# Kernel tuning notes

Hardware: AMD Instinct MI355X
Metric: run time of the kernel (lower is better)

The kernel has to match this reference:

```python
import jax, jax.numpy as jnp
import numpy as np

DIM = 512
HEADS = 8
D_HEAD = 64
INNER_FF = 4 * DIM  # 2048
EPS = 1e-5
SCALE = D_HEAD ** -0.5


def _layernorm(x, w, b):
    x = x.astype(jnp.float32)
    mu = jnp.mean(x, axis=-1, keepdims=True)
    var = jnp.mean(jnp.square(x - mu), axis=-1, keepdims=True)
    return (x - mu) * jax.lax.rsqrt(var + EPS) * w + b


def _l2_attn(x, wq, bq, wv, bv, wo, bo):
    # x: [B, N, DIM]. k = q (context is ignored in the original module).
    b, n, _ = x.shape
    q = (x @ wq + bq).reshape(b, n, HEADS, D_HEAD).transpose(0, 2, 1, 3)  # b h n d
    v = (x @ wv + bv).reshape(b, n, HEADS, D_HEAD).transpose(0, 2, 1, 3)
    q = q.astype(jnp.float32)
    AB = jnp.einsum('bhid,bhjd->bhij', q, q)          # [b,h,n,n]
    AA = jnp.sum(jnp.square(q), axis=-1)               # [b,h,n]
    sim = -(AA[..., :, None] - 2.0 * AB + AA[..., None, :]) * SCALE
    attn = jax.nn.softmax(sim, axis=-1)
    out = jnp.einsum('bhij,bhjd->bhid', attn, v)       # [b,h,n,d]
    out = out.transpose(0, 2, 1, 3).reshape(b, n, HEADS * D_HEAD)
    return out @ wo + bo


def _geglu_ff(x, w1, b1, w2, b2):
    h = x @ w1 + b1                      # [B, N, 2*INNER_FF]
    a, gate = jnp.split(h, 2, axis=-1)
    return (a * jax.nn.gelu(gate, approximate=False)) @ w2 + b2


def setup_inputs() -> dict:
    key = jax.random.key(0)
    ks = jax.random.split(key, 24)
    s = 0.02
    d = {'x': jax.random.normal(ks[0], (4, 2048, DIM), jnp.float32)}
    # layernorms
    d['sa_norm_w'] = jnp.ones((DIM,), jnp.float32)
    d['sa_norm_b'] = jnp.zeros((DIM,), jnp.float32)
    d['ca_norm_w'] = jnp.ones((DIM,), jnp.float32)
    d['ca_norm_b'] = jnp.zeros((DIM,), jnp.float32)
    d['ff_norm_w'] = jnp.ones((DIM,), jnp.float32)
    d['ff_norm_b'] = jnp.zeros((DIM,), jnp.float32)
    # attn1 (self)
    d['a1_wq'] = jax.random.normal(ks[1], (DIM, DIM), jnp.float32) * s
    d['a1_bq'] = jnp.zeros((DIM,), jnp.float32)
    d['a1_wv'] = jax.random.normal(ks[2], (DIM, DIM), jnp.float32) * s
    d['a1_bv'] = jnp.zeros((DIM,), jnp.float32)
    d['a1_wo'] = jax.random.normal(ks[3], (DIM, DIM), jnp.float32) * s
    d['a1_bo'] = jnp.zeros((DIM,), jnp.float32)
    # attn2 (cross, but k=q and v from x in original code)
    d['a2_wq'] = jax.random.normal(ks[4], (DIM, DIM), jnp.float32) * s
    d['a2_bq'] = jnp.zeros((DIM,), jnp.float32)
    d['a2_wv'] = jax.random.normal(ks[5], (DIM, DIM), jnp.float32) * s
    d['a2_bv'] = jnp.zeros((DIM,), jnp.float32)
    d['a2_wo'] = jax.random.normal(ks[6], (DIM, DIM), jnp.float32) * s
    d['a2_bo'] = jnp.zeros((DIM,), jnp.float32)
    # GEGLU FFN
    d['ff_w1'] = jax.random.normal(ks[7], (DIM, 2 * INNER_FF), jnp.float32) * s
    d['ff_b1'] = jnp.zeros((2 * INNER_FF,), jnp.float32)
    d['ff_w2'] = jax.random.normal(ks[8], (INNER_FF, DIM), jnp.float32) * s
    d['ff_b2'] = jnp.zeros((DIM,), jnp.float32)
    return d


def reference(x, sa_norm_w, sa_norm_b, ca_norm_w, ca_norm_b, ff_norm_w, ff_norm_b,
              a1_wq, a1_bq, a1_wv, a1_bv, a1_wo, a1_bo,
              a2_wq, a2_bq, a2_wv, a2_bv, a2_wo, a2_bo,
              ff_w1, ff_b1, ff_w2, ff_b2):
    x = _l2_attn(_layernorm(x, sa_norm_w, sa_norm_b), a1_wq, a1_bq, a1_wv, a1_bv, a1_wo, a1_bo) + x
    x = _l2_attn(_layernorm(x, ca_norm_w, ca_norm_b), a2_wq, a2_bq, a2_wv, a2_bv, a2_wo, a2_bo) + x
    x = _geglu_ff(_layernorm(x, ff_norm_w, ff_norm_b), ff_w1, ff_b1, ff_w2, ff_b2) + x
    return x
```

## Files before the change

### kernel.cpp

```cpp
#include <hip/hip_runtime.h>
#include <hip/hip_bf16.h>


typedef short bf16x8 __attribute__((ext_vector_type(8)));
typedef float f32x4 __attribute__((ext_vector_type(4)));
typedef unsigned short u16;
typedef unsigned int u32;

__device__ __forceinline__ float bf2f(u16 u) {
    return __uint_as_float(((u32)u) << 16);
}
__device__ __forceinline__ u16 f2bf(float f) {
    u32 u = __float_as_uint(f);
    u32 rb = ((u >> 16) & 1u) + 0x7fffu;
    return (u16)((u + rb) >> 16);
}
__device__ __forceinline__ float gelu_fast(float x) {
    float y = 1.5957691216f * (x + 0.044715f * x * x * x);
    return x / (1.f + __expf(-y));
}
__device__ __forceinline__ void gl2lds16(const u16* g, u16* l) {
    __builtin_amdgcn_global_load_lds(
        (const __attribute__((address_space(1))) void*)(unsigned long long)(uintptr_t)g,
        (__attribute__((address_space(3))) void*)(unsigned long long)(uintptr_t)l,
        16, 0, 0);
}

struct TArgs {
    const float* src[8];
    u16* dst[8];
    int R[8], C[8];
    int start[9];
};
__global__ __launch_bounds__(256) void transpose_multi(TArgs a) {
    __shared__ float tile[32][33];
    int bid = blockIdx.x;
    int s = 0;
    while (bid >= a.start[s + 1]) s++;
    int local = bid - a.start[s];
    int R = a.R[s], C = a.C[s];
    int tx = C >> 5;
    int bx = local % tx, by = local / tx;
    const float* in = a.src[s];
    u16* out = a.dst[s];
    int t = threadIdx.x;
    int c = t & 31, r0 = (t >> 5) * 4;
#pragma unroll
    for (int i = 0; i < 4; i++)
        tile[r0 + i][c] = in[(size_t)(by * 32 + r0 + i) * C + bx * 32 + c];
    __syncthreads();
#pragma unroll
    for (int i = 0; i < 4; i++)
        out[(size_t)(bx * 32 + r0 + i) * R + by * 32 + c] = f2bf(tile[c][r0 + i]);
}

__global__ __launch_bounds__(256) void ln_kernel(const float* __restrict__ x,
                                                 const float* __restrict__ w,
                                                 const float* __restrict__ b,
                                                 u16* __restrict__ out) {
    int row = blockIdx.x, t = threadIdx.x;
    const float* xr = x + (size_t)row * 512;
    float2 v = *(const float2*)(xr + t * 2);
    float s1 = v.x + v.y;
    float s2 = v.x * v.x + v.y * v.y;
#pragma unroll
    for (int m = 1; m < 64; m <<= 1) {
        s1 += __shfl_xor(s1, m);
        s2 += __shfl_xor(s2, m);
    }
    __shared__ float r1[4], r2[4];
    int wave = t >> 6, lane = t & 63;
    if (lane == 0) { r1[wave] = s1; r2[wave] = s2; }
    __syncthreads();
    float tot1 = r1[0] + r1[1] + r1[2] + r1[3];
    float tot2 = r2[0] + r2[1] + r2[2] + r2[3];
    float mu = tot1 * (1.f / 512.f);
    float var = tot2 * (1.f / 512.f) - mu * mu;
    float rs = rsqrtf(var + 1e-5f);
    float2 wv = *(const float2*)(w + t * 2);
    float2 bv = *(const float2*)(b + t * 2);
    float o0 = (v.x - mu) * rs * wv.x + bv.x;
    float o1 = (v.y - mu) * rs * wv.y + bv.y;
    u32 pack = (u32)f2bf(o0) | ((u32)f2bf(o1) << 16);
    *(u32*)(out + (size_t)row * 512 + t * 2) = pack;
}

__global__ __launch_bounds__(256) void gemm_ff1(const u16* __restrict__ A,
                                                const u16* __restrict__ BT,
                                                const float* __restrict__ bias,
                                                u16* __restrict__ gout,
                                                int K) {
    __shared__ u16 As[2][128 * 32];
    __shared__ u16 Bs[2][128 * 32];
    int t = threadIdx.x;
    int wave = t >> 6, lane = t & 63, quad = lane >> 4, l16 = lane & 15;
    int m0 = blockIdx.x * 128, n0 = blockIdx.y * 64;
    f32x4 aacc[2][4], gacc[2][4];
#pragma unroll
    for (int i = 0; i < 2; i++)
#pragma unroll
        for (int j = 0; j < 4; j++) {
            aacc[i][j] = (f32x4){0.f, 0.f, 0.f, 0.f};
            gacc[i][j] = (f32x4){0.f, 0.f, 0.f, 0.f};
        }
    const u16* Ag = A + (size_t)(m0 + wave * 32 + (lane >> 2)) * K + (lane & 3) * 8;
    int brow = (wave < 2) ? (n0 + wave * 32) : (2048 + n0 + (wave - 2) * 32);
    const u16* Bg = BT + (size_t)(brow + (lane >> 2)) * K + (lane & 3) * 8;
    int lo = wave * 32 * 32;
    const size_t rstep = (size_t)16 * K;
    gl2lds16(Ag, &As[0][lo]);
    gl2lds16(Ag + rstep, &As[0][lo + 16 * 32]);
    gl2lds16(Bg, &Bs[0][lo]);
    gl2lds16(Bg + rstep, &Bs[0][lo + 16 * 32]);
    int buf = 0;
    for (int k0 = 0; k0 < K; k0 += 32, buf ^= 1) {
        int kn = (k0 + 32 < K) ? (k0 + 32) : k0;
        int nb = buf ^ 1;
        asm volatile("s_waitcnt lgkmcnt(0)\n\ts_barrier" ::: "memory");
        gl2lds16(Ag + kn, &As[nb][lo]);
        gl2lds16(Ag + kn + rstep, &As[nb][lo + 16 * 32]);
        gl2lds16(Bg + kn, &Bs[nb][lo]);
        gl2lds16(Bg + kn + rstep, &Bs[nb][lo + 16 * 32]);
        asm volatile("s_waitcnt vmcnt(4)\n\ts_barrier" ::: "memory");
        bf16x8 a[2];
#pragma unroll
        for (int i = 0; i < 2; i++)
            a[i] = *(const bf16x8*)&As[buf][(wave * 32 + i * 16 + l16) * 32 + quad * 8];
#pragma unroll
        for (int j = 0; j < 4; j++) {
            bf16x8 ba = *(const bf16x8*)&Bs[buf][(j * 16 + l16) * 32 + quad * 8];
            bf16x8 bg = *(const bf16x8*)&Bs[buf][(64 + j * 16 + l16) * 32 + quad * 8];
#pragma unroll
            for (int i = 0; i < 2; i++) {
                aacc[i][j] = __builtin_amdgcn_mfma_f32_16x16x32_bf16(a[i], ba, aacc[i][j], 0, 0, 0);
                gacc[i][j] = __builtin_amdgcn_mfma_f32_16x16x32_bf16(a[i], bg, gacc[i][j], 0, 0, 0);
            }
        }
    }
    asm volatile("s_waitcnt vmcnt(0)" ::: "memory");
    int row_base = m0 + wave * 32 + quad * 4;
#pragma unroll
    for (int j = 0; j < 4; j++) {
        int col = n0 + j * 16 + l16;
        float ba = bias[col];
        float bg = bias[2048 + col];
#pragma unroll
        for (int i = 0; i < 2; i++) {
#pragma unroll
            for (int r = 0; r < 4; r++) {
                int row = row_base + i * 16 + r;
                float av = aacc[i][j][r] + ba;
                float gv = gacc[i][j][r] + bg;
                gout[(size_t)row * 2048 + col] = f2bf(av * gelu_fast(gv));
            }
        }
    }
}

template <int MODE>
__global__ __launch_bounds__(256) void gemm_rect(const u16* __restrict__ A,
                                                 const u16* __restrict__ BT,
                                                 const float* __restrict__ bias,
                                                 const float* __restrict__ bias2,
                                                 const float* __restrict__ res,
                                                 float* __restrict__ outf,
                                                 u16* __restrict__ outb,
                                                 u16* __restrict__ outb2,
                                                 float* __restrict__ aa,
                                                 int M, int N, int K) {
    __shared__ u16 As[2][128 * 32];
    __shared__ u16 Bs[2][64 * 32];
    int t = threadIdx.x;
    int wave = t >> 6, lane = t & 63, quad = lane >> 4, l16 = lane & 15;
    int m0 = blockIdx.x * 128, n0 = blockIdx.y * 64;
    f32x4 acc[2][4];
#pragma unroll
    for (int i = 0; i < 2; i++)
#pragma unroll
        for (int j = 0; j < 4; j++) acc[i][j] = (f32x4){0.f, 0.f, 0.f, 0.f};
    const u16* Ag = A + (size_t)(m0 + wave * 32 + (lane >> 2)) * K + (lane & 3) * 8;
    const u16* Bg = BT + (size_t)(n0 + wave * 16 + (lane >> 2)) * K + (lane & 3) * 8;
    int loA = wave * 32 * 32;
    int loB = wave * 16 * 32;
    const size_t rstep = (size_t)16 * K;
    gl2lds16(Ag, &As[0][loA]);
    gl2lds16(Ag + rstep, &As[0][loA + 16 * 32]);
    gl2lds16(Bg, &Bs[0][loB]);
    int buf = 0;
    for (int k0 = 0; k0 < K; k0 += 32, buf ^= 1) {
        int kn = (k0 + 32 < K) ? (k0 + 32) : k0;
        int nb = buf ^ 1;
        asm volatile("s_waitcnt lgkmcnt(0)\n\ts_barrier" ::: "memory");
        gl2lds16(Ag + kn, &As[nb][loA]);
        gl2lds16(Ag + kn + rstep, &As[nb][loA + 16 * 32]);
        gl2lds16(Bg + kn, &Bs[nb][loB]);
        asm volatile("s_waitcnt vmcnt(3)\n\ts_barrier" ::: "memory");
        bf16x8 a[2], b[4];
#pragma unroll
        for (int i = 0; i < 2; i++)
            a[i] = *(const bf16x8*)&As[buf][(wave * 32 + i * 16 + l16) * 32 + quad * 8];
#pragma unroll
        for (int j = 0; j < 4; j++)
            b[j] = *(const bf16x8*)&Bs[buf][(j * 16 + l16) * 32 + quad * 8];
#pragma unroll
        for (int i = 0; i < 2; i++)
#pragma unroll
            for (int j = 0; j < 4; j++)
                acc[i][j] = __builtin_amdgcn_mfma_f32_16x16x32_bf16(a[i], b[j], acc[i][j], 0, 0, 0);
    }
    asm volatile("s_waitcnt vmcnt(0)" ::: "memory");
    int row_base = m0 + wave * 32 + quad * 4;
    float ssq[2][4];
#pragma unroll
    for (int i = 0; i < 2; i++)
#pragma unroll
        for (int r = 0; r < 4; r++) ssq[i][r] = 0.f;
#pragma unroll
    for (int j = 0; j < 4; j++) {
        int col = n0 + j * 16 + l16;
        float bv;
        if (MODE == 4) bv = (col < 512) ? bias[col] : bias2[col - 512];
        else bv = bias[col];
#pragma unroll
        for (int i = 0; i < 2; i++) {
            int rowA = row_base + i * 16;
            if (MODE == 4) {
                if (col < 512) {
                    int hh = col >> 6, d = col & 63;
#pragma unroll
                    for (int r = 0; r < 4; r++) {
                        int row = rowA + r;
                        float v = acc[i][j][r] + bv;
                        ssq[i][r] += v * v;
                        outb[((size_t)((row >> 11) * 8 + hh) * 2048 + (row & 2047)) * 64 + d] = f2bf(v);
                    }
                } else {
                    int c2 = col - 512;
                    int hh = c2 >> 6, d = c2 & 63;
                    int n = rowA & 2047;
                    int a4 = (n >> 2) & 7;
                    int ncol = (n & ~31) + ((a4 & 3) << 3) + ((a4 >> 2) << 2);
                    u32 plo = (u32)f2bf(acc[i][j][0] + bv) | ((u32)f2bf(acc[i][j][1] + bv) << 16);
                    u32 phi = (u32)f2bf(acc[i][j][2] + bv) | ((u32)f2bf(acc[i][j][3] + bv) << 16);
                    uint2 pk; pk.x = plo; pk.y = phi;
                    *(uint2*)&outb2[((size_t)((rowA >> 11) * 8 + hh) * 64 + d) * 2048 + ncol] = pk;
                }
            } else {
#pragma unroll
                for (int r = 0; r < 4; r++) {
                    size_t idx = (size_t)(rowA + r) * N + col;
                    outf[idx] = acc[i][j][r] + bv + res[idx];
                }
            }
        }
    }
    if (MODE == 4 && n0 < 512) {
        int hh = n0 >> 6;
#pragma unroll
        for (int i = 0; i < 2; i++) {
#pragma unroll
            for (int r = 0; r < 4; r++) {
                float s = ssq[i][r];
                s += __shfl_xor(s, 1); s += __shfl_xor(s, 2);
                s += __shfl_xor(s, 4); s += __shfl_xor(s, 8);
                if (l16 == 0) {
                    int row = row_base + i * 16 + r;
                    aa[(size_t)((row >> 11) * 8 + hh) * 2048 + (row & 2047)] = s * 0.18033688f;
                }
            }
        }
    }
}

__global__ __launch_bounds__(256) void attn_mfma(const u16* __restrict__ qbuf,
                                                 const u16* __restrict__ vtp,
                                                 const float* __restrict__ aas,
                                                 u16* __restrict__ out) {
    __shared__ u16 L[2][16384];
    int bid = blockIdx.x;
    int bh = bid & 31;
    int itile = bid >> 5;
    const u16* qb = qbuf + (size_t)bh * 2048 * 64;
    const u16* vtb = vtp + (size_t)bh * 64 * 2048;
    const float* aab = aas + (size_t)bh * 2048;
    int t = threadIdx.x;
    int wave = t >> 6, lane = t & 63, quad = lane >> 4, l16 = lane & 15;
    int sw7 = l16 & 7;
    int ibase = itile * 128 + wave * 32;

    bf16x8 qf[2][2];
    f32x4 O[2][4];
    float lr[2] = {0.f, 0.f};
#pragma unroll
    for (int st = 0; st < 2; st++) {
        const u16* qr = qb + (size_t)(ibase + st * 16 + l16) * 64;
        qf[st][0] = *(const bf16x8*)(qr + quad * 8);
        qf[st][1] = *(const bf16x8*)(qr + 32 + quad * 8);
#pragma unroll
        for (int nt = 0; nt < 4; nt++) O[st][nt] = (f32x4){0.f, 0.f, 0.f, 0.f};
    }

    int qrow[4], qcs[4], qwof[4], vrow[4], vsl[4], vwof[4];
#pragma unroll
    for (int k = 0; k < 4; k++) {
        int s = t + k * 256;
        qrow[k] = s >> 3; qcs[k] = s & 7;
        qwof[k] = qrow[k] * 64 + 8 * (qcs[k] ^ (qrow[k] & 7));
        vrow[k] = s >> 4; vsl[k] = s & 15;
        vwof[k] = 8192 + vrow[k] * 128 + 8 * ((vsl[k] & 8) | ((vsl[k] & 7) ^ (vrow[k] & 7)));
    }
#pragma unroll
    for (int k = 0; k < 4; k++) {
        *(uint4*)&L[0][qwof[k]] = *(const uint4*)(qb + (size_t)qrow[k] * 64 + qcs[k] * 8);
        *(uint4*)&L[0][vwof[k]] = *(const uint4*)(vtb + (size_t)vrow[k] * 2048 + vsl[k] * 8);
    }
    __syncthreads();

    const float C0 = 0.36067376f;
    for (int it = 0; it < 16; ++it) {
        int cur = it & 1;
        int j0 = it << 7;
        uint4 pq[4], pv[4];
        bool more = (it + 1 < 16);
        if (more) {
            int j0n = j0 + 128;
#pragma unroll
            for (int k = 0; k < 4; k++) {
                pq[k] = *(const uint4*)(qb + (size_t)(j0n + qrow[k]) * 64 + qcs[k] * 8);
                pv[k] = *(const uint4*)(vtb + (size_t)vrow[k] * 2048 + j0n + vsl[k] * 8);
            }
        }
        const u16* Q = &L[cur][0];
        const u16* V = &L[cur][8192];
#pragma unroll
        for (int c = 0; c < 4; c++) {
            int r10 = c * 32 + l16, r20 = c * 32 + 16 + l16;
            bf16x8 a10 = *(const bf16x8*)&Q[r10 * 64 + 8 * (quad ^ sw7)];
            bf16x8 a11 = *(const bf16x8*)&Q[r10 * 64 + 8 * ((4 + quad) ^ sw7)];
            bf16x8 a20 = *(const bf16x8*)&Q[r20 * 64 + 8 * (quad ^ sw7)];
            bf16x8 a21 = *(const bf16x8*)&Q[r20 * 64 + 8 * ((4 + quad) ^ sw7)];
            f32x4 s0[2], s1[2];
            __builtin_amdgcn_s_setprio(1);
#pragma unroll
            for (int st = 0; st < 2; st++) {
                f32x4 z = {0.f, 0.f, 0.f, 0.f};
                s0[st] = __builtin_amdgcn_mfma_f32_16x16x32_bf16(a10, qf[st][0], z, 0, 0, 0);
                s0[st] = __builtin_amdgcn_mfma_f32_16x16x32_bf16(a11, qf[st][1], s0[st], 0, 0, 0);
                s1[st] = __builtin_amdgcn_mfma_f32_16x16x32_bf16(a20, qf[st][0], z, 0, 0, 0);
                s1[st] = __builtin_amdgcn_mfma_f32_16x16x32_bf16(a21, qf[st][1], s1[st], 0, 0, 0);
            }
            __builtin_amdgcn_s_setprio(0);
            float4 aav0 = *(const float4*)(aab + j0 + c * 32 + quad * 4);
            float4 aav1 = *(const float4*)(aab + j0 + c * 32 + 16 + quad * 4);
            bf16x8 pa[2];
#pragma unroll
            for (int st = 0; st < 2; st++) {
                float p0 = __builtin_amdgcn_exp2f(fmaf(s0[st][0], C0, -aav0.x));
                float p1 = __builtin_amdgcn_exp2f(fmaf(s0[st][1], C0, -aav0.y));
                float p2 = __builtin_amdgcn_exp2f(fmaf(s0[st][2], C0, -aav0.z));
                float p3 = __builtin_amdgcn_exp2f(fmaf(s0[st][3], C0, -aav0.w));
                float p4 = __builtin_amdgcn_exp2f(fmaf(s1[st][0], C0, -aav1.x));
                float p5 = __builtin_amdgcn_exp2f(fmaf(s1[st][1], C0, -aav1.y));
                float p6 = __builtin_amdgcn_exp2f(fmaf(s1[st][2], C0, -aav1.z));
                float p7 = __builtin_amdgcn_exp2f(fmaf(s1[st][3], C0, -aav1.w));
                lr[st] += (p0 + p1 + p2 + p3) + (p4 + p5 + p6 + p7);
                u32* pu = (u32*)&pa[st];
                pu[0] = __builtin_amdgcn_perm(__float_as_uint(p1), __float_as_uint(p0), 0x07060302u);
                pu[1] = __builtin_amdgcn_perm(__float_as_uint(p3), __float_as_uint(p2), 0x07060302u);
                pu[2] = __builtin_amdgcn_perm(__float_as_uint(p5), __float_as_uint(p4), 0x07060302u);
                pu[3] = __builtin_amdgcn_perm(__float_as_uint(p7), __float_as_uint(p6), 0x07060302u);
            }
            __builtin_amdgcn_s_setprio(1);
#pragma unroll
            for (int nt = 0; nt < 4; nt++) {
                int sl = c * 4 + quad;
                bf16x8 vf = *(const bf16x8*)&V[(nt * 16 + l16) * 128 + 8 * ((sl & 8) | ((sl & 7) ^ sw7))];
                O[0][nt] = __builtin_amdgcn_mfma_f32_16x16x32_bf16(pa[0], vf, O[0][nt], 0, 0, 0);
                O[1][nt] = __builtin_amdgcn_mfma_f32_16x16x32_bf16(pa[1], vf, O[1][nt], 0, 0, 0);
            }
            __builtin_amdgcn_s_setprio(0);
        }
        if (more) {
            u16* D = &L[cur ^ 1][0];
#pragma unroll
            for (int k = 0; k < 4; k++) {
                *(uint4*)&D[qwof[k]] = pq[k];
                *(uint4*)&D[vwof[k]] = pv[k];
            }
        }
        __syncthreads();
    }

    int b = bh >> 3, h = bh & 7;
#pragma unroll
    for (int st = 0; st < 2; st++) {
        float l = lr[st];
        l += __shfl_xor(l, 16);
        l += __shfl_xor(l, 32);
        float inv = 1.f / l;
#pragma unroll
        for (int r = 0; r < 4; r++) {
            float invr = __shfl(inv, quad * 4 + r);
            size_t row = (size_t)(b * 2048 + ibase + st * 16 + quad * 4 + r);
            u16* o = out + row * 512 + h * 64 + l16;
            o[0]  = f2bf(O[st][0][r] * invr);
            o[16] = f2bf(O[st][1][r] * invr);
            o[32] = f2bf(O[st][2][r] * invr);
            o[48] = f2bf(O[st][3][r] * invr);
        }
    }
}

extern "C" void kernel_launch(void* const* d_in, const int* in_sizes, int n_in,
                              void* d_out, int out_size, void* d_ws, size_t ws_size,
                              hipStream_t stream) {
    const float* x      = (const float*)d_in[0];
    const float* sa_w   = (const float*)d_in[1];
    const float* sa_b   = (const float*)d_in[2];
    const float* ca_w   = (const float*)d_in[3];
    const float* ca_b   = (const float*)d_in[4];
    const float* ffn_w  = (const float*)d_in[5];
    const float* ffn_b  = (const float*)d_in[6];
    const float* a1_wq  = (const float*)d_in[7];
    const float* a1_bq  = (const float*)d_in[8];
    const float* a1_wv  = (const float*)d_in[9];
    const float* a1_bv  = (const float*)d_in[10];
    const float* a1_wo  = (const float*)d_in[11];
    const float* a1_bo  = (const float*)d_in[12];
    const float* a2_wq  = (const float*)d_in[13];
    const float* a2_bq  = (const float*)d_in[14];
    const float* a2_wv  = (const float*)d_in[15];
    const float* a2_bv  = (const float*)d_in[16];
    const float* a2_wo  = (const float*)d_in[17];
    const float* a2_bo  = (const float*)d_in[18];
    const float* ff_w1  = (const float*)d_in[19];
    const float* ff_b1  = (const float*)d_in[20];
    const float* ff_w2  = (const float*)d_in[21];
    const float* ff_b2  = (const float*)d_in[22];

    char* ws = (char*)d_ws;
    const size_t MB = 1ull << 20;
    float* x_res   = (float*)(ws);
    u16* xn        = (u16*)(ws + 16 * MB);
    u16* wT_a1qv   = (u16*)(ws + 24 * MB);
    u16* wT_a2qv   = (u16*)(ws + 25 * MB);
    u16* wT_a1o    = (u16*)(ws + 26 * MB);
    u16* wT_a2o    = (u16*)(ws + 26 * MB + 512 * 1024);
    u16* wT_ff1    = (u16*)(ws + 27 * MB);
    u16* wT_ff2    = (u16*)(ws + 31 * MB);
    u16* qbuf      = (u16*)(ws + 34 * MB);
    u16* vtp       = (u16*)(ws + 42 * MB);
    float* aab     = (float*)(ws + 50 * MB);
    u16* attn_o    = (u16*)(ws + 51 * MB);
    u16* gbuf      = (u16*)(ws + 60 * MB);

    (void)in_sizes; (void)n_in; (void)out_size; (void)ws_size;

    TArgs ta;
    ta.src[0] = a1_wq; ta.dst[0] = wT_a1qv;               ta.R[0] = 512;  ta.C[0] = 512;
    ta.src[1] = a1_wv; ta.dst[1] = wT_a1qv + 512 * 512;   ta.R[1] = 512;  ta.C[1] = 512;
    ta.src[2] = a2_wq; ta.dst[2] = wT_a2qv;               ta.R[2] = 512;  ta.C[2] = 512;
    ta.src[3] = a2_wv; ta.dst[3] = wT_a2qv + 512 * 512;   ta.R[3] = 512;  ta.C[3] = 512;
    ta.src[4] = a1_wo; ta.dst[4] = wT_a1o;                ta.R[4] = 512;  ta.C[4] = 512;
    ta.src[5] = a2_wo; ta.dst[5] = wT_a2o;                ta.R[5] = 512;  ta.C[5] = 512;
    ta.src[6] = ff_w1; ta.dst[6] = wT_ff1;                ta.R[6] = 512;  ta.C[6] = 4096;
    ta.src[7] = ff_w2; ta.dst[7] = wT_ff2;                ta.R[7] = 2048; ta.C[7] = 512;
    ta.start[0] = 0;
    for (int s = 0; s < 8; s++)
        ta.start[s + 1] = ta.start[s] + (ta.C[s] >> 5) * (ta.R[s] >> 5);
    transpose_multi<<<ta.start[8], 256, 0, stream>>>(ta);

    ln_kernel<<<8192, 256, 0, stream>>>(x, sa_w, sa_b, xn);
    gemm_rect<4><<<dim3(64, 16), 256, 0, stream>>>(xn, wT_a1qv, a1_bq, a1_bv, nullptr, nullptr, qbuf, vtp, aab, 8192, 1024, 512);
    attn_mfma<<<512, 256, 0, stream>>>(qbuf, vtp, aab, attn_o);
    gemm_rect<2><<<dim3(64, 8), 256, 0, stream>>>(attn_o, wT_a1o, a1_bo, nullptr, x, x_res, nullptr, nullptr, nullptr, 8192, 512, 512);

    ln_kernel<<<8192, 256, 0, stream>>>(x_res, ca_w, ca_b, xn);
    gemm_rect<4><<<dim3(64, 16), 256, 0, stream>>>(xn, wT_a2qv, a2_bq, a2_bv, nullptr, nullptr, qbuf, vtp, aab, 8192, 1024, 512);
    attn_mfma<<<512, 256, 0, stream>>>(qbuf, vtp, aab, attn_o);
    gemm_rect<2><<<dim3(64, 8), 256, 0, stream>>>(attn_o, wT_a2o, a2_bo, nullptr, x_res, x_res, nullptr, nullptr, nullptr, 8192, 512, 512);

    ln_kernel<<<8192, 256, 0, stream>>>(x_res, ffn_w, ffn_b, xn);
    gemm_ff1<<<dim3(64, 32), 256, 0, stream>>>(xn, wT_ff1, ff_b1, gbuf, 512);
    gemm_rect<2><<<dim3(64, 8), 256, 0, stream>>>(gbuf, wT_ff2, ff_b2, nullptr, x_res, (float*)d_out, nullptr, nullptr, nullptr, 8192, 512, 2048);
}
```

Before: 399.4 us.

## Split attention key range in two and add a combine kernel

The attention kernel now splits the 2048-key range into two halves, launching 1024 blocks instead of 512, each streaming 64-key tiles with a smaller LDS footprint. Each block writes unnormalized fp32 partial outputs and row sums to workspace. A new combine kernel adds the two halves, normalizes, and writes bf16 output. The aim is better CU occupancy and more parallelism (512 blocks on 256 CUs), paid for with extra fp32 partial-result traffic and an extra launch per attention layer.

```diff
diff --git a/kernel.cpp b/kernel.cpp
--- a/kernel.cpp
+++ b/kernel.cpp
@@ -275,11 +275,14 @@
 __global__ __launch_bounds__(256) void attn_mfma(const u16* __restrict__ qbuf,
                                                  const u16* __restrict__ vtp,
                                                  const float* __restrict__ aas,
-                                                 u16* __restrict__ out) {
-    __shared__ u16 L[2][16384];
+                                                 float* __restrict__ opart,
+                                                 float* __restrict__ lrpart) {
+    __shared__ u16 L[2][8192];
     int bid = blockIdx.x;
     int bh = bid & 31;
-    int itile = bid >> 5;
+    int js = (bid >> 5) & 1;
+    int itile = bid >> 6;
+    int jbase = js << 10;
     const u16* qb = qbuf + (size_t)bh * 2048 * 64;
     const u16* vtb = vtp + (size_t)bh * 64 * 2048;
     const float* aab = aas + (size_t)bh * 2048;
@@ -300,40 +303,42 @@
         for (int nt = 0; nt < 4; nt++) O[st][nt] = (f32x4){0.f, 0.f, 0.f, 0.f};
     }
 
-    int qrow[4], qcs[4], qwof[4], vrow[4], vsl[4], vwof[4];
-#pragma unroll
-    for (int k = 0; k < 4; k++) {
-        int s = t + k * 256;
-        qrow[k] = s >> 3; qcs[k] = s & 7;
-        qwof[k] = qrow[k] * 64 + 8 * (qcs[k] ^ (qrow[k] & 7));
-        vrow[k] = s >> 4; vsl[k] = s & 15;
-        vwof[k] = 8192 + vrow[k] * 128 + 8 * ((vsl[k] & 8) | ((vsl[k] & 7) ^ (vrow[k] & 7)));
-    }
-#pragma unroll
-    for (int k = 0; k < 4; k++) {
-        *(uint4*)&L[0][qwof[k]] = *(const uint4*)(qb + (size_t)qrow[k] * 64 + qcs[k] * 8);
-        *(uint4*)&L[0][vwof[k]] = *(const uint4*)(vtb + (size_t)vrow[k] * 2048 + vsl[k] * 8);
+    int r1 = t >> 3, cs = t & 7;
+    int swof = 8 * (cs ^ (r1 & 7));
+    int qwof1 = r1 * 64 + swof;
+    int qwof2 = (r1 + 32) * 64 + swof;
+    int vwof1 = 4096 + qwof1;
+    int vwof2 = 4096 + qwof2;
+
+    {
+        uint4 pq1 = *(const uint4*)(qb + (size_t)(jbase + r1) * 64 + cs * 8);
+        uint4 pq2 = *(const uint4*)(qb + (size_t)(jbase + r1 + 32) * 64 + cs * 8);
+        uint4 pv1 = *(const uint4*)(vtb + (size_t)r1 * 2048 + jbase + cs * 8);
+        uint4 pv2 = *(const uint4*)(vtb + (size_t)(r1 + 32) * 2048 + jbase + cs * 8);
+        *(uint4*)&L[0][qwof1] = pq1;
+        *(uint4*)&L[0][qwof2] = pq2;
+        *(uint4*)&L[0][vwof1] = pv1;
+        *(uint4*)&L[0][vwof2] = pv2;
     }
     __syncthreads();
 
     const float C0 = 0.36067376f;
     for (int it = 0; it < 16; ++it) {
         int cur = it & 1;
-        int j0 = it << 7;
-        uint4 pq[4], pv[4];
+        int j0 = jbase + (it << 6);
+        uint4 pq1, pq2, pv1, pv2;
         bool more = (it + 1 < 16);
         if (more) {
-            int j0n = j0 + 128;
-#pragma unroll
-            for (int k = 0; k < 4; k++) {
-                pq[k] = *(const uint4*)(qb + (size_t)(j0n + qrow[k]) * 64 + qcs[k] * 8);
-                pv[k] = *(const uint4*)(vtb + (size_t)vrow[k] * 2048 + j0n + vsl[k] * 8);
-            }
+            int j0n = j0 + 64;
+            pq1 = *(const uint4*)(qb + (size_t)(j0n + r1) * 64 + cs * 8);
+            pq2 = *(const uint4*)(qb + (size_t)(j0n + r1 + 32) * 64 + cs * 8);
+            pv1 = *(const uint4*)(vtb + (size_t)r1 * 2048 + j0n + cs * 8);
+            pv2 = *(const uint4*)(vtb + (size_t)(r1 + 32) * 2048 + j0n + cs * 8);
         }
         const u16* Q = &L[cur][0];
-        const u16* V = &L[cur][8192];
-#pragma unroll
-        for (int c = 0; c < 4; c++) {
+        const u16* V = &L[cur][4096];
+#pragma unroll
+        for (int c = 0; c < 2; c++) {
             int r10 = c * 32 + l16, r20 = c * 32 + 16 + l16;
             bf16x8 a10 = *(const bf16x8*)&Q[r10 * 64 + 8 * (quad ^ sw7)];
             bf16x8 a11 = *(const bf16x8*)&Q[r10 * 64 + 8 * ((4 + quad) ^ sw7)];
@@ -373,8 +378,7 @@
             __builtin_amdgcn_s_setprio(1);
 #pragma unroll
             for (int nt = 0; nt < 4; nt++) {
-                int sl = c * 4 + quad;
-                bf16x8 vf = *(const bf16x8*)&V[(nt * 16 + l16) * 128 + 8 * ((sl & 8) | ((sl & 7) ^ sw7))];
+                bf16x8 vf = *(const bf16x8*)&V[(nt * 16 + l16) * 64 + 8 * ((c * 4 + quad) ^ sw7)];
                 O[0][nt] = __builtin_amdgcn_mfma_f32_16x16x32_bf16(pa[0], vf, O[0][nt], 0, 0, 0);
                 O[1][nt] = __builtin_amdgcn_mfma_f32_16x16x32_bf16(pa[1], vf, O[1][nt], 0, 0, 0);
             }
@@ -382,33 +386,62 @@
         }
         if (more) {
             u16* D = &L[cur ^ 1][0];
-#pragma unroll
-            for (int k = 0; k < 4; k++) {
-                *(uint4*)&D[qwof[k]] = pq[k];
-                *(uint4*)&D[vwof[k]] = pv[k];
-            }
+            *(uint4*)&D[qwof1] = pq1;
+            *(uint4*)&D[qwof2] = pq2;
+            *(uint4*)&D[vwof1] = pv1;
+            *(uint4*)&D[vwof2] = pv2;
         }
         __syncthreads();
     }
 
-    int b = bh >> 3, h = bh & 7;
+    size_t pslot = (size_t)js * 32 + bh;
 #pragma unroll
     for (int st = 0; st < 2; st++) {
         float l = lr[st];
         l += __shfl_xor(l, 16);
         l += __shfl_xor(l, 32);
-        float inv = 1.f / l;
+        if (lane < 16)
+            lrpart[pslot * 2048 + ibase + st * 16 + l16] = l;
+        float* ob = opart + (pslot * 2048 + ibase + st * 16 + quad * 4) * 64 + l16;
 #pragma unroll
         for (int r = 0; r < 4; r++) {
-            float invr = __shfl(inv, quad * 4 + r);
-            size_t row = (size_t)(b * 2048 + ibase + st * 16 + quad * 4 + r);
-            u16* o = out + row * 512 + h * 64 + l16;
-            o[0]  = f2bf(O[st][0][r] * invr);
-            o[16] = f2bf(O[st][1][r] * invr);
-            o[32] = f2bf(O[st][2][r] * invr);
-            o[48] = f2bf(O[st][3][r] * invr);
-        }
-    }
+            float* o = ob + (size_t)r * 64;
+            o[0]  = O[st][0][r];
+            o[16] = O[st][1][r];
+            o[32] = O[st][2][r];
+            o[48] = O[st][3][r];
+        }
+    }
+}
+
+__global__ __launch_bounds__(256) void attn_combine(const float* __restrict__ opart,
+                                                    const float* __restrict__ lrpart,
+                                                    u16* __restrict__ out) {
+    int t = threadIdx.x;
+    int rl = t >> 3, d0 = (t & 7) * 8;
+    int rg = blockIdx.x * 32 + rl;
+    int bh = rg >> 11, i = rg & 2047;
+    const float* o0 = opart + ((size_t)bh * 2048 + i) * 64 + d0;
+    const float* o1 = o0 + (size_t)32 * 2048 * 64;
+    float lr = lrpart[(size_t)bh * 2048 + i] +
+               lrpart[(size_t)32 * 2048 + (size_t)bh * 2048 + i];
+    float inv = 1.f / lr;
+    float4 a0 = *(const float4*)o0;
+    float4 a1 = *(const float4*)(o0 + 4);
+    float4 b0 = *(const float4*)o1;
+    float4 b1 = *(const float4*)(o1 + 4);
+    int b = bh >> 3, h = bh & 7;
+    u16* op = out + ((size_t)(b * 2048 + i)) * 512 + h * 64 + d0;
+    u16 r[8];
+    r[0] = f2bf((a0.x + b0.x) * inv);
+    r[1] = f2bf((a0.y + b0.y) * inv);
+    r[2] = f2bf((a0.z + b0.z) * inv);
+    r[3] = f2bf((a0.w + b0.w) * inv);
+    r[4] = f2bf((a1.x + b1.x) * inv);
+    r[5] = f2bf((a1.y + b1.y) * inv);
+    r[6] = f2bf((a1.z + b1.z) * inv);
+    r[7] = f2bf((a1.w + b1.w) * inv);
+    *(uint4*)op = *(uint4*)r;
 }
 
 extern "C" void kernel_launch(void* const* d_in, const int* in_sizes, int n_in,
@@ -451,8 +484,10 @@
     u16* qbuf      = (u16*)(ws + 34 * MB);
     u16* vtp       = (u16*)(ws + 42 * MB);
     float* aab     = (float*)(ws + 50 * MB);
+    float* lrp     = (float*)(ws + 50 * MB + 256 * 1024);
     u16* attn_o    = (u16*)(ws + 51 * MB);
     u16* gbuf      = (u16*)(ws + 60 * MB);
+    float* opart   = (float*)(ws + 60 * MB);
 
     (void)in_sizes; (void)n_in; (void)out_size; (void)ws_size;
 
@@ -472,12 +507,14 @@
 
     ln_kernel<<<8192, 256, 0, stream>>>(x, sa_w, sa_b, xn);
     gemm_rect<4><<<dim3(64, 16), 256, 0, stream>>>(xn, wT_a1qv, a1_bq, a1_bv, nullptr, nullptr, qbuf, vtp, aab, 8192, 1024, 512);
-    attn_mfma<<<512, 256, 0, stream>>>(qbuf, vtp, aab, attn_o);
+    attn_mfma<<<1024, 256, 0, stream>>>(qbuf, vtp, aab, opart, lrp);
+    attn_combine<<<2048, 256, 0, stream>>>(opart, lrp, attn_o);
     gemm_rect<2><<<dim3(64, 8), 256, 0, stream>>>(attn_o, wT_a1o, a1_bo, nullptr, x, x_res, nullptr, nullptr, nullptr, 8192, 512, 512);
 
     ln_kernel<<<8192, 256, 0, stream>>>(x_res, ca_w, ca_b, xn);
     gemm_rect<4><<<dim3(64, 16), 256, 0, stream>>>(xn, wT_a2qv, a2_bq, a2_bv, nullptr, nullptr, qbuf, vtp, aab, 8192, 1024, 512);
-    attn_mfma<<<512, 256, 0, stream>>>(qbuf, vtp, aab, attn_o);
+    attn_mfma<<<1024, 256, 0, stream>>>(qbuf, vtp, aab, opart, lrp);
+    attn_combine<<<2048, 256, 0, stream>>>(opart, lrp, attn_o);
     gemm_rect<2><<<dim3(64, 8), 256, 0, stream>>>(attn_o, wT_a2o, a2_bo, nullptr, x_res, x_res, nullptr, nullptr, nullptr, 8192, 512, 512);
 
     ln_kernel<<<8192, 256, 0, stream>>>(x_res, ffn_w, ffn_b, xn);
```

Measured after the change: 417.7 us. +4.6%, slower.

## Load key-side Q fragments directly from global with register prefetch instead of LDS

Applied to the files above, without the earlier changes.

The attention kernel no longer stages the key-side Q tile in shared memory. Each wave now reads its MFMA A-operand fragments straight from global memory (through the cache) and prefetches the next 32-row chunk into registers one step ahead. LDS then holds only the V tile. This removes the LDS writes and reads for Q and halves the shared-memory footprint. The cost is redundant global/L2 reads across the four waves, more live registers, and exposed global-load latency inside the inner loop.

```diff
diff --git a/kernel.cpp b/kernel.cpp
--- a/kernel.cpp
+++ b/kernel.cpp
@@ -300,54 +300,54 @@
         for (int nt = 0; nt < 4; nt++) O[st][nt] = (f32x4){0.f, 0.f, 0.f, 0.f};
     }
 
-    int qrow[4], qcs[4], qwof[4], vrow[4], vsl[4], vwof[4];
+    int vrow[4], vsl[4], vwof[4];
 #pragma unroll
     for (int k = 0; k < 4; k++) {
         int s = t + k * 256;
-        qrow[k] = s >> 3; qcs[k] = s & 7;
-        qwof[k] = qrow[k] * 64 + 8 * (qcs[k] ^ (qrow[k] & 7));
         vrow[k] = s >> 4; vsl[k] = s & 15;
-        vwof[k] = 8192 + vrow[k] * 128 + 8 * ((vsl[k] & 8) | ((vsl[k] & 7) ^ (vrow[k] & 7)));
-    }
-#pragma unroll
-    for (int k = 0; k < 4; k++) {
-        *(uint4*)&L[0][qwof[k]] = *(const uint4*)(qb + (size_t)qrow[k] * 64 + qcs[k] * 8);
+        vwof[k] = vrow[k] * 128 + 8 * ((vsl[k] & 8) | ((vsl[k] & 7) ^ (vrow[k] & 7)));
+    }
+#pragma unroll
+    for (int k = 0; k < 4; k++)
         *(uint4*)&L[0][vwof[k]] = *(const uint4*)(vtb + (size_t)vrow[k] * 2048 + vsl[k] * 8);
-    }
+
+    const u16* qjb = qb + (size_t)l16 * 64 + quad * 8;
+    bf16x8 aq0 = *(const bf16x8*)(qjb);
+    bf16x8 aq1 = *(const bf16x8*)(qjb + 32);
+    bf16x8 aq2 = *(const bf16x8*)(qjb + 16 * 64);
+    bf16x8 aq3 = *(const bf16x8*)(qjb + 16 * 64 + 32);
     __syncthreads();
 
     const float C0 = 0.36067376f;
     for (int it = 0; it < 16; ++it) {
         int cur = it & 1;
         int j0 = it << 7;
-        uint4 pq[4], pv[4];
+        uint4 pv[4];
         bool more = (it + 1 < 16);
         if (more) {
             int j0n = j0 + 128;
 #pragma unroll
-            for (int k = 0; k < 4; k++) {
-                pq[k] = *(const uint4*)(qb + (size_t)(j0n + qrow[k]) * 64 + qcs[k] * 8);
+            for (int k = 0; k < 4; k++)
                 pv[k] = *(const uint4*)(vtb + (size_t)vrow[k] * 2048 + j0n + vsl[k] * 8);
-            }
-        }
-        const u16* Q = &L[cur][0];
-        const u16* V = &L[cur][8192];
+        }
+        const u16* V = &L[cur][0];
 #pragma unroll
         for (int c = 0; c < 4; c++) {
-            int r10 = c * 32 + l16, r20 = c * 32 + 16 + l16;
-            bf16x8 a10 = *(const bf16x8*)&Q[r10 * 64 + 8 * (quad ^ sw7)];
-            bf16x8 a11 = *(const bf16x8*)&Q[r10 * 64 + 8 * ((4 + quad) ^ sw7)];
-            bf16x8 a20 = *(const bf16x8*)&Q[r20 * 64 + 8 * (quad ^ sw7)];
-            bf16x8 a21 = *(const bf16x8*)&Q[r20 * 64 + 8 * ((4 + quad) ^ sw7)];
+            int jn = (c < 3) ? (j0 + (c + 1) * 32) : (more ? j0 + 128 : 0);
+            const u16* qn = qjb + (size_t)jn * 64;
+            bf16x8 nq0 = *(const bf16x8*)(qn);
+            bf16x8 nq1 = *(const bf16x8*)(qn + 32);
+            bf16x8 nq2 = *(const bf16x8*)(qn + 16 * 64);
+            bf16x8 nq3 = *(const bf16x8*)(qn + 16 * 64 + 32);
             f32x4 s0[2], s1[2];
             __builtin_amdgcn_s_setprio(1);
 #pragma unroll
             for (int st = 0; st < 2; st++) {
                 f32x4 z = {0.f, 0.f, 0.f, 0.f};
-                s0[st] = __builtin_amdgcn_mfma_f32_16x16x32_bf16(a10, qf[st][0], z, 0, 0, 0);
-                s0[st] = __builtin_amdgcn_mfma_f32_16x16x32_bf16(a11, qf[st][1], s0[st], 0, 0, 0);
-                s1[st] = __builtin_amdgcn_mfma_f32_16x16x32_bf16(a20, qf[st][0], z, 0, 0, 0);
-                s1[st] = __builtin_amdgcn_mfma_f32_16x16x32_bf16(a21, qf[st][1], s1[st], 0, 0, 0);
+                s0[st] = __builtin_amdgcn_mfma_f32_16x16x32_bf16(aq0, qf[st][0], z, 0, 0, 0);
+                s0[st] = __builtin_amdgcn_mfma_f32_16x16x32_bf16(aq1, qf[st][1], s0[st], 0, 0, 0);
+                s1[st] = __builtin_amdgcn_mfma_f32_16x16x32_bf16(aq2, qf[st][0], z, 0, 0, 0);
+                s1[st] = __builtin_amdgcn_mfma_f32_16x16x32_bf16(aq3, qf[st][1], s1[st], 0, 0, 0);
             }
             __builtin_amdgcn_s_setprio(0);
             float4 aav0 = *(const float4*)(aab + j0 + c * 32 + quad * 4);
@@ -379,14 +379,13 @@
                 O[1][nt] = __builtin_amdgcn_mfma_f32_16x16x32_bf16(pa[1], vf, O[1][nt], 0, 0, 0);
             }
             __builtin_amdgcn_s_setprio(0);
+            aq0 = nq0; aq1 = nq1; aq2 = nq2; aq3 = nq3;
         }
         if (more) {
             u16* D = &L[cur ^ 1][0];
 #pragma unroll
-            for (int k = 0; k < 4; k++) {
-                *(uint4*)&D[qwof[k]] = pq[k];
+            for (int k = 0; k < 4; k++)
                 *(uint4*)&D[vwof[k]] = pv[k];
-            }
         }
         __syncthreads();
     }
```

New measurement: 441.0 us. +10.4%, slower.
